# Kernel optimization log

Measured on AMD Instinct MI355X. Metric: run time of the kernel, lower is better.

The kernel has to match this reference:

```python
import jax, jax.numpy as jnp
import numpy as np

# RoIAlign 2D config (matches init_kwargs)
OUT_H, OUT_W = 7, 7
SPATIAL_SCALE = 0.25
S = 2  # sampling_ratio: S x S sample points per output bin
N, C, H, W = 4, 256, 200, 200
R = 512


def setup_inputs() -> dict:
    key = jax.random.key(0)
    k1, k2, k3, k4, k5 = jax.random.split(key, 5)
    features = jax.random.normal(k1, (N, C, H, W), dtype=jnp.float32)
    # rois in image coordinates (image is H/scale = 800 px): (batch_idx, x1, y1, x2, y2)
    img = H / SPATIAL_SCALE
    b = jax.random.randint(k2, (R,), 0, N).astype(jnp.float32)
    xy1 = jax.random.uniform(k3, (R, 2), dtype=jnp.float32, maxval=img - 96.0)
    wh = jax.random.uniform(k4, (R, 2), dtype=jnp.float32, minval=16.0, maxval=96.0)
    rois = jnp.concatenate([b[:, None], xy1, xy1 + wh], axis=1)  # [R,5]
    return {"features": features, "rois": rois}


def _axis_weights(start, bin_size, out_size, limit):
    """Per-axis sample coords -> (low/high indices [R,out*S,2], lerp weights [R,out*S,2]).
    Matches mmdet/torchvision RoIAlign CUDA kernel semantics."""
    # sample coordinate: start + (i + 0.5) * bin / S  ==  start + ph*bin + (iy+0.5)*bin/S
    i = (jnp.arange(out_size * S, dtype=jnp.float32) + 0.5) / S
    y = start[:, None] + i[None, :] * bin_size[:, None]          # [R, out*S]
    valid = (y >= -1.0) & (y <= limit)                            # kernel: skip if y<-1 or y>H
    yc = jnp.clip(y, 0.0, limit - 1.0)
    yl = jnp.floor(yc).astype(jnp.int32)                          # in [0, H-1]
    yh = jnp.minimum(yl + 1, limit - 1)
    l = yc - yl.astype(jnp.float32)                               # 0 at the top edge, as in kernel
    w = jnp.stack([1.0 - l, l], axis=-1) * valid[..., None].astype(jnp.float32)  # [R,out*S,2]
    idx = jnp.stack([yl, yh], axis=-1)                            # [R,out*S,2]
    return idx, w


def reference(features, rois):
    # order=1 (bilinear) path of RoIAlign2DFunction
    b = rois[:, 0].astype(jnp.int32)                              # [R]
    x1, y1, x2, y2 = (rois[:, k] * SPATIAL_SCALE for k in (1, 2, 3, 4))
    roi_w = jnp.maximum(x2 - x1, 1.0)
    roi_h = jnp.maximum(y2 - y1, 1.0)
    bin_w = roi_w / OUT_W
    bin_h = roi_h / OUT_H

    yidx, wy = _axis_weights(y1, bin_h, OUT_H, H)                 # [R,Hs,2]
    xidx, wx = _axis_weights(x1, bin_w, OUT_W, W)                 # [R,Ws,2]

    nhwc = jnp.transpose(features, (0, 2, 3, 1))                  # [N,H,W,C]
    # gather 2x2 bilinear neighbors for every sample point: [R,Hs,Ws,2,2,C]
    vals = nhwc[b[:, None, None, None, None],
                yidx[:, :, None, :, None],
                xidx[:, None, :, None, :]]
    samples = jnp.einsum('rhwabc,rha,rwb->rhwc', vals, wy, wx)    # [R,Hs,Ws,C]
    Hs, Ws = OUT_H * S, OUT_W * S
    pooled = samples.reshape(R, OUT_H, S, OUT_W, S, C).mean(axis=(2, 4))  # avg over S*S points
    return jnp.transpose(pooled, (0, 3, 1, 2))                    # [R,C,out_h,out_w]
```

## Files before the change

kernel.cpp:

```cpp
#include <hip/hip_runtime.h>


#define OH 7
#define OW 7
#define NSAMP 14
#define NB 4
#define CH 256
#define FH 200
#define FW 200
#define NR 512
#define CCH 8
#define NCHUNK (CH / CCH)
#define MAXF 25
#define MAXSEG 7
#define MAXTOTP 177
#define BLK 256

__global__ __launch_bounds__(BLK) void roialign_fwd(
    const float* __restrict__ feat,
    const float* __restrict__ rois,
    float* __restrict__ out)
{
    __shared__ float tile[CCH * MAXTOTP * 4];
    __shared__ int   s_il[2][NSAMP];
    __shared__ int   s_ih[2][NSAMP];
    __shared__ float s_w0[2][NSAMP];
    __shared__ float s_w1[2][NSAMP];

    const int block = blockIdx.x;
    const int r     = block >> 5;
    const int chunk = block & (NCHUNK - 1);
    const int c0    = chunk * CCH;
    const int tid   = threadIdx.x;

    const int   b  = (int)rois[r * 5 + 0];
    const float x1 = rois[r * 5 + 1] * 0.25f;
    const float y1 = rois[r * 5 + 2] * 0.25f;
    const float x2 = rois[r * 5 + 3] * 0.25f;
    const float y2 = rois[r * 5 + 4] * 0.25f;
    const float roi_w = fmaxf(x2 - x1, 1.0f);
    const float roi_h = fmaxf(y2 - y1, 1.0f);
    const float bw = roi_w * (1.0f / OW);
    const float bh = roi_h * (1.0f / OH);

    if (tid < 2 * NSAMP) {
        const int axis = tid >= NSAMP;
        const int i    = tid - axis * NSAMP;
        const float start = axis ? x1 : y1;
        const float bsz   = axis ? bw : bh;
        const float pos   = start + (i + 0.5f) * 0.5f * bsz;
        const float valid = (pos >= -1.0f && pos <= 200.0f) ? 1.0f : 0.0f;
        const float pc    = fminf(fmaxf(pos, 0.0f), 199.0f);
        const int   il    = (int)floorf(pc);
        const int   ih    = min(il + 1, 199);
        const float l     = pc - (float)il;
        s_il[axis][i] = il;
        s_ih[axis][i] = ih;
        s_w0[axis][i] = (1.0f - l) * valid;
        s_w1[axis][i] = l * valid;
    }
    __syncthreads();

    const int ylo = s_il[0][0];
    const int xlo = s_il[1][0];
    const int fh = min(s_ih[0][NSAMP - 1] - ylo + 1, MAXF);
    const int fw = min(s_ih[1][NSAMP - 1] - xlo + 1, MAXF);
    const int x0   = xlo & ~3;
    const int nseg = ((xlo - x0) + fw + 3) >> 2;
    const int rstr = nseg << 2;
    const int tot  = fh * nseg;
    const int totp = tot + ((1 - tot) & 7);
    const int pstr = totp << 2;

    {
        const int lane = tid & 63;
        const int wave = tid >> 6;
        const float* gend = feat + (size_t)NB * CH * FH * FW - 4;
        #pragma unroll
        for (int k = 0; k < 2; k++) {
            const int c = (wave << 1) | k;
            const float* gplane =
                feat + ((size_t)(b * CH + c0 + c) * FH + ylo) * FW + x0;
            float* lplane = tile + c * pstr;
            #pragma unroll
            for (int t = 0; t < 3; t++) {
                const int s = (t << 6) + lane;
                if (s < tot) {
                    const int ys = (unsigned)s / (unsigned)nseg;
                    const int sx = s - ys * nseg;
                    const float* g = gplane + ys * FW + (sx << 2);
                    if (g > gend) g = gend;
                    float* l = lplane + (s << 2);
                    __builtin_amdgcn_global_load_lds(
                        (const __attribute__((address_space(1))) void*)g,
                        (__attribute__((address_space(3))) void*)l,
                        16, 0, 0);
                }
            }
        }
    }
    __syncthreads();

    const int cl   = tid & (CCH - 1);
    const int slot = tid >> 3;
    const float* tc = tile + cl * pstr;

    for (int bin = slot; bin < OH * OW; bin += BLK / CCH) {
        const int ph = bin / OW;
        const int pw = bin - ph * OW;
        float acc = 0.0f;
        #pragma unroll
        for (int sy = 0; sy < 2; sy++) {
            const int gy = ph * 2 + sy;
            const int rowl = (s_il[0][gy] - ylo) * rstr;
            const int rowh = (s_ih[0][gy] - ylo) * rstr;
            const float wy0 = s_w0[0][gy];
            const float wy1 = s_w1[0][gy];
            #pragma unroll
            for (int sx = 0; sx < 2; sx++) {
                const int gx = pw * 2 + sx;
                const int ixl = s_il[1][gx] - x0;
                const int ixh = s_ih[1][gx] - x0;
                const float wx0 = s_w0[1][gx];
                const float wx1 = s_w1[1][gx];
                acc += wy0 * (wx0 * tc[rowl + ixl] + wx1 * tc[rowl + ixh])
                     + wy1 * (wx0 * tc[rowh + ixl] + wx1 * tc[rowh + ixh]);
            }
        }
        out[(size_t)(r * CH + c0 + cl) * (OH * OW) + bin] = acc * 0.25f;
    }
}

extern "C" void kernel_launch(void* const* d_in, const int* in_sizes, int n_in,
                              void* d_out, int out_size, void* d_ws, size_t ws_size,
                              hipStream_t stream) {
    const float* feat = (const float*)d_in[0];
    const float* rois = (const float*)d_in[1];
    float* out = (float*)d_out;
    roialign_fwd<<<NR * NCHUNK, BLK, 0, stream>>>(feat, rois, out);
}
```

Before: 246.5 us.

## Sort ROIs by spatial locality and remap blocks for L2 reuse

Adds a single-block bitonic sort kernel that orders ROIs by batch, y and x, and remaps block IDs so that consecutive blocks handle spatially nearby ROIs for the same channel chunk, with chunks spread across XCDs. The aim is to raise L2/MALL hit rates for overlapping feature windows. The LDS tile now uses a fixed row stride of 32 floats, which drops the integer division in the load loop but uses more LDS per block and may lower occupancy. It also adds a second kernel launch and depends on the workspace for the permutation.

```diff
diff --git a/kernel.cpp b/kernel.cpp
--- a/kernel.cpp
+++ b/kernel.cpp
@@ -12,24 +12,54 @@
 #define CCH 8
 #define NCHUNK (CH / CCH)
 #define MAXF 25
-#define MAXSEG 7
-#define MAXTOTP 177
+#define PSTRMAX (MAXF * 32 + 4)
 #define BLK 256
+
+__global__ __launch_bounds__(NR) void roi_sort(
+    const float* __restrict__ rois, int* __restrict__ perm)
+{
+    __shared__ unsigned key[NR];
+    const int t = threadIdx.x;
+    {
+        const int   b  = (int)rois[t * 5 + 0];
+        const float x1 = rois[t * 5 + 1] * 0.25f;
+        const float y1 = rois[t * 5 + 2] * 0.25f;
+        const int qy = min(255, max(0, (int)y1));
+        const int qx = min(255, max(0, (int)x1));
+        key[t] = ((unsigned)b << 27) | ((unsigned)qy << 18)
+               | ((unsigned)qx << 9) | (unsigned)t;
+    }
+    for (int k = 2; k <= NR; k <<= 1) {
+        for (int j = k >> 1; j > 0; j >>= 1) {
+            __syncthreads();
+            const int ixj = t ^ j;
+            if (ixj > t) {
+                const unsigned a = key[t], c = key[ixj];
+                const bool asc = ((t & k) == 0);
+                if ((a > c) == asc) { key[t] = c; key[ixj] = a; }
+            }
+        }
+    }
+    __syncthreads();
+    perm[t] = (int)(key[t] & (NR - 1u));
+}
 
 __global__ __launch_bounds__(BLK) void roialign_fwd(
     const float* __restrict__ feat,
     const float* __restrict__ rois,
+    const int*   __restrict__ perm,
     float* __restrict__ out)
 {
-    __shared__ float tile[CCH * MAXTOTP * 4];
+    __shared__ float tile[CCH * PSTRMAX];
     __shared__ int   s_il[2][NSAMP];
     __shared__ int   s_ih[2][NSAMP];
     __shared__ float s_w0[2][NSAMP];
     __shared__ float s_w1[2][NSAMP];
 
-    const int block = blockIdx.x;
-    const int r     = block >> 5;
-    const int chunk = block & (NCHUNK - 1);
+    const int bid   = blockIdx.x;
+    const int nid   = ((bid & 7) << 11) | (bid >> 3);
+    const int chunk = nid >> 9;
+    const int r     = perm[nid & (NR - 1)];
     const int c0    = chunk * CCH;
     const int tid   = threadIdx.x;
 
@@ -67,10 +97,7 @@
     const int fw = min(s_ih[1][NSAMP - 1] - xlo + 1, MAXF);
     const int x0   = xlo & ~3;
     const int nseg = ((xlo - x0) + fw + 3) >> 2;
-    const int rstr = nseg << 2;
-    const int tot  = fh * nseg;
-    const int totp = tot + ((1 - tot) & 7);
-    const int pstr = totp << 2;
+    const int pstr = (fh << 5) + 4;
 
     {
         const int lane = tid & 63;
@@ -83,17 +110,16 @@
                 feat + ((size_t)(b * CH + c0 + c) * FH + ylo) * FW + x0;
             float* lplane = tile + c * pstr;
             #pragma unroll
-            for (int t = 0; t < 3; t++) {
-                const int s = (t << 6) + lane;
-                if (s < tot) {
-                    const int ys = (unsigned)s / (unsigned)nseg;
-                    const int sx = s - ys * nseg;
+            for (int t = 0; t < 4; t++) {
+                const int s  = (t << 6) + lane;
+                const int ys = s >> 3;
+                const int sx = s & 7;
+                if (ys < fh && sx < nseg) {
                     const float* g = gplane + ys * FW + (sx << 2);
                     if (g > gend) g = gend;
-                    float* l = lplane + (s << 2);
                     __builtin_amdgcn_global_load_lds(
                         (const __attribute__((address_space(1))) void*)g,
-                        (__attribute__((address_space(3))) void*)l,
+                        (__attribute__((address_space(3))) void*)(lplane + (s << 2)),
                         16, 0, 0);
                 }
             }
@@ -112,8 +138,8 @@
         #pragma unroll
         for (int sy = 0; sy < 2; sy++) {
             const int gy = ph * 2 + sy;
-            const int rowl = (s_il[0][gy] - ylo) * rstr;
-            const int rowh = (s_ih[0][gy] - ylo) * rstr;
+            const int rowl = (s_il[0][gy] - ylo) << 5;
+            const int rowh = (s_ih[0][gy] - ylo) << 5;
             const float wy0 = s_w0[0][gy];
             const float wy1 = s_w1[0][gy];
             #pragma unroll
@@ -137,5 +163,7 @@
     const float* feat = (const float*)d_in[0];
     const float* rois = (const float*)d_in[1];
     float* out = (float*)d_out;
-    roialign_fwd<<<NR * NCHUNK, BLK, 0, stream>>>(feat, rois, out);
+    int* perm = (int*)d_ws;
+    roi_sort<<<1, NR, 0, stream>>>(rois, perm);
+    roialign_fwd<<<NR * NCHUNK, BLK, 0, stream>>>(feat, rois, perm, out);
 }
```

After: 242.3 us. About the same (-1.7%).
